# Kernel optimization log

Measured on AMD Instinct MI355X. Metric: run time of the kernel, lower is better.

## Reference

```python
import jax, jax.numpy as jnp
import numpy as np

B, S, DIM = 2, 2048, 2048
N_HEADS, N_KV = 16, 4
HEAD_DIM = DIM // N_HEADS
THETA = 10000.0


def _rope_tables(seq, half, theta):
    inv_freq = 1.0 / (theta ** (jnp.arange(0, half, dtype=jnp.float32) / half))
    t = jnp.arange(seq, dtype=jnp.float32)
    freqs = jnp.outer(t, inv_freq)  # (seq, half)
    return jnp.cos(freqs), jnp.sin(freqs)


def setup_inputs() -> dict:
    key = jax.random.key(0)
    ks = jax.random.split(key, 6)
    cos, sin = _rope_tables(S, HEAD_DIM // 2, THETA)
    scale_in = 1.0 / np.sqrt(DIM)
    return {
        "x": jax.random.normal(ks[0], (B, S, DIM), dtype=jnp.float32),
        "cos": cos,
        "sin": sin,
        "attn_mask": jax.random.randint(ks[1], (B, 1, 1, S), 0, 2) > 0,
        "Wq": jax.random.normal(ks[2], (N_HEADS * HEAD_DIM, DIM), dtype=jnp.float32) * scale_in,
        "Wk": jax.random.normal(ks[3], (N_KV * HEAD_DIM, DIM), dtype=jnp.float32) * scale_in,
        "Wv": jax.random.normal(ks[4], (N_KV * HEAD_DIM, DIM), dtype=jnp.float32) * scale_in,
        "Wo": jax.random.normal(ks[5], (DIM, N_HEADS * HEAD_DIM), dtype=jnp.float32) * scale_in,
    }


def _apply_rope(x, cos, sin):
    # x: (B, H, S, D); cos/sin: (S, D//2)
    D = x.shape[-1]
    x1, x2 = x[..., : D // 2], x[..., D // 2:]
    c = cos[None, None, : x.shape[2]]
    s = sin[None, None, : x.shape[2]]
    return jnp.concatenate([x1 * c - x2 * s, x1 * s + x2 * c], axis=-1)


def reference(x, cos, sin, attn_mask, Wq, Wk, Wv, Wo):
    b, s, _ = x.shape
    d = 2 * cos.shape[1]
    h = Wq.shape[0] // d
    kvh = Wk.shape[0] // d
    g = h // kvh  # query heads per KV head

    q = (x @ Wq.T).reshape(b, s, h, d).transpose(0, 2, 1, 3)     # (B,H,S,D)
    k = (x @ Wk.T).reshape(b, s, kvh, d).transpose(0, 2, 1, 3)   # (B,KV,S,D)
    v = (x @ Wv.T).reshape(b, s, kvh, d).transpose(0, 2, 1, 3)

    q = _apply_rope(q, cos, sin)
    k = _apply_rope(k, cos, sin)

    # Grouped attention without materializing repeated KV.
    qg = q.reshape(b, kvh, g, s, d)
    scores = jnp.einsum("bkgsd,bktd->bkgst", qg, k) / jnp.sqrt(jnp.asarray(d, q.dtype))
    mask = attn_mask[:, :, None]  # (B,1,1,1,S) broadcast over (B,KV,G,S,T)
    scores = jnp.where(mask, -jnp.inf, scores)
    attn = jax.nn.softmax(scores, axis=-1)
    out = jnp.einsum("bkgst,bktd->bkgsd", attn, v)
    out = out.reshape(b, h, s, d).transpose(0, 2, 1, 3).reshape(b, s, h * d)
    return out @ Wo.T
```

## Files before the change

### kernel.cpp

```cpp
#include <hip/hip_runtime.h>

typedef __attribute__((ext_vector_type(8))) short s16x8;
typedef __attribute__((ext_vector_type(4))) float f32x4;

#define B_    2
#define S_    2048
#define DIM_  2048
#define H_    16
#define KVH_  4
#define HD_   128
#define NQKV  3072

static __device__ __forceinline__ unsigned short f2bf(float f) {
  unsigned int u = __float_as_uint(f);
  u += 0x7fff + ((u >> 16) & 1);
  return (unsigned short)(u >> 16);
}
static __device__ __forceinline__ float bf2f(unsigned short h) {
  return __uint_as_float(((unsigned int)h) << 16);
}
static __device__ __forceinline__ float fexp2(float x) {
#if __has_builtin(__builtin_amdgcn_exp2f)
  return __builtin_amdgcn_exp2f(x);
#else
  return exp2f(x);
#endif
}

__global__ __launch_bounds__(256) void cast_all(const float* __restrict__ x,
                                                const float* __restrict__ wq,
                                                const float* __restrict__ wk,
                                                const float* __restrict__ wv,
                                                const float* __restrict__ wo,
                                                unsigned short* __restrict__ xb,
                                                unsigned short* __restrict__ wqkv,
                                                unsigned short* __restrict__ wob) {
  int blk = blockIdx.x;
  const float* s;
  unsigned short* d;
  int rel;
  if (blk < 4096)      { s = x;  d = xb;             rel = blk; }
  else if (blk < 6144) { s = wq; d = wqkv;           rel = blk - 4096; }
  else if (blk < 6656) { s = wk; d = wqkv + 4194304; rel = blk - 6144; }
  else if (blk < 7168) { s = wv; d = wqkv + 5242880; rel = blk - 6656; }
  else                 { s = wo; d = wob;            rel = blk - 7168; }
  int i = (rel * 256 + threadIdx.x) * 8;
  float4 a = *(const float4*)(s + i);
  float4 b = *(const float4*)(s + i + 4);
  uint4 o;
  o.x = (unsigned)f2bf(a.x) | ((unsigned)f2bf(a.y) << 16);
  o.y = (unsigned)f2bf(a.z) | ((unsigned)f2bf(a.w) << 16);
  o.z = (unsigned)f2bf(b.x) | ((unsigned)f2bf(b.y) << 16);
  o.w = (unsigned)f2bf(b.z) | ((unsigned)f2bf(b.w) << 16);
  *(uint4*)(d + i) = o;
}

__global__ __launch_bounds__(256) void scan_mask(const int* __restrict__ mask,
                                                 int* __restrict__ posmap,
                                                 int* __restrict__ cnts) {
  int b = blockIdx.x;
  __shared__ int a0[S_], a1[S_];
  int tid = threadIdx.x;
  for (int i = tid; i < S_; i += 256) a0[i] = (mask[b * S_ + i] == 0) ? 1 : 0;
  __syncthreads();
  int* src = a0;
  int* dst = a1;
  for (int off = 1; off < S_; off <<= 1) {
    for (int i = tid; i < S_; i += 256)
      dst[i] = src[i] + (i >= off ? src[i - off] : 0);
    __syncthreads();
    int* t = src; src = dst; dst = t;
  }
  for (int i = tid; i < S_; i += 256)
    posmap[b * S_ + i] = (mask[b * S_ + i] == 0) ? (src[i] - 1) : -1;
  if (tid == 0) cnts[b] = src[S_ - 1];
}

template <bool BF16OUT>
__global__ __launch_bounds__(256) void gemm_bt(const unsigned short* __restrict__ A,
                                               const unsigned short* __restrict__ Bw,
                                               void* __restrict__ Cp, int N, int K) {
  __shared__ __align__(16) unsigned short As[128 * 32];
  __shared__ __align__(16) unsigned short Bs[128 * 32];
  const int tid = threadIdx.x;
  const int gx = gridDim.x;
  const int lin = blockIdx.y * gx + blockIdx.x;
  const int cpx = (gx * gridDim.y) >> 3;
  const int nlin = (lin & 7) * cpx + (lin >> 3);
  const int n0 = (nlin % gx) * 128, m0 = (nlin / gx) * 128;
  const int w = tid >> 6, l = tid & 63;
  const int wr = w >> 1, wc = w & 1;
  const int lo = l & 15, hi = l >> 4;
  f32x4 acc[4][4] = {};
  const int KT = K >> 5;
  for (int kt = 0; kt < KT; ++kt) {
    const int k0 = kt << 5;
    __syncthreads();
#pragma unroll
    for (int c = 0; c < 2; ++c) {
      int idx = tid + c * 256;
      int row = idx >> 2, ko = (idx & 3) << 3;
      __builtin_amdgcn_global_load_lds(
          (__attribute__((address_space(1))) void*)(A + (size_t)(m0 + row) * K + k0 + ko),
          (__attribute__((address_space(3))) void*)(As + idx * 8), 16, 0, 0);
      __builtin_amdgcn_global_load_lds(
          (__attribute__((address_space(1))) void*)(Bw + (size_t)(n0 + row) * K + k0 + ko),
          (__attribute__((address_space(3))) void*)(Bs + idx * 8), 16, 0, 0);
    }
    asm volatile("s_waitcnt vmcnt(0)" ::: "memory");
    __syncthreads();
    s16x8 af[4], bfr[4];
#pragma unroll
    for (int mi = 0; mi < 4; ++mi)
      af[mi] = *(const s16x8*)(As + (wr * 64 + mi * 16 + lo) * 32 + hi * 8);
#pragma unroll
    for (int ni = 0; ni < 4; ++ni)
      bfr[ni] = *(const s16x8*)(Bs + (wc * 64 + ni * 16 + lo) * 32 + hi * 8);
#pragma unroll
    for (int mi = 0; mi < 4; ++mi)
#pragma unroll
      for (int ni = 0; ni < 4; ++ni)
        acc[mi][ni] = __builtin_amdgcn_mfma_f32_16x16x32_bf16(af[mi], bfr[ni], acc[mi][ni], 0, 0, 0);
  }
#pragma unroll
  for (int mi = 0; mi < 4; ++mi) {
#pragma unroll
    for (int ni = 0; ni < 4; ++ni) {
      int col = n0 + wc * 64 + ni * 16 + lo;
      int rowb = m0 + wr * 64 + mi * 16 + hi * 4;
#pragma unroll
      for (int r = 0; r < 4; ++r) {
        float v = acc[mi][ni][r];
        if (BF16OUT)
          ((unsigned short*)Cp)[(size_t)(rowb + r) * N + col] = f2bf(v);
        else
          ((float*)Cp)[(size_t)(rowb + r) * N + col] = v;
      }
    }
  }
}

__global__ __launch_bounds__(256) void rope_q(const unsigned short* __restrict__ QKV,
                                              const float* __restrict__ ctab,
                                              const float* __restrict__ stab,
                                              unsigned short* __restrict__ dst, float scale) {
  int gid = blockIdx.x * 256 + threadIdx.x;
  int i = gid & 63;
  int rest = gid >> 6;
  int h = rest & 15;
  int s = (rest >> 4) & (S_ - 1);
  int b = rest >> 15;
  const unsigned short* row = QKV + (size_t)(b * S_ + s) * NQKV + h * HD_;
  float x1 = bf2f(row[i]), x2 = bf2f(row[i + 64]);
  float c = ctab[s * 64 + i], sn = stab[s * 64 + i];
  unsigned short* drow = dst + ((size_t)(b * H_ + h) * S_ + s) * HD_;
  drow[i] = f2bf((x1 * c - x2 * sn) * scale);
  drow[i + 64] = f2bf((x1 * sn + x2 * c) * scale);
}

__global__ __launch_bounds__(256) void rope_k(const unsigned short* __restrict__ QKV,
                                              const float* __restrict__ ctab,
                                              const float* __restrict__ stab,
                                              const int* __restrict__ posmap,
                                              unsigned short* __restrict__ dst) {
  int gid = blockIdx.x * 256 + threadIdx.x;
  int i = gid & 63;
  int rest = gid >> 6;
  int h = rest & 3;
  int s = (rest >> 2) & (S_ - 1);
  int b = rest >> 13;
  int sp = posmap[b * S_ + s];
  if (sp < 0) return;
  const unsigned short* row = QKV + (size_t)(b * S_ + s) * NQKV + DIM_ + h * HD_;
  float x1 = bf2f(row[i]), x2 = bf2f(row[i + 64]);
  float c = ctab[s * 64 + i], sn = stab[s * 64 + i];
  unsigned short* drow = dst + ((size_t)(b * KVH_ + h) * S_ + sp) * HD_;
  drow[i] = f2bf(x1 * c - x2 * sn);
  drow[i + 64] = f2bf(x1 * sn + x2 * c);
}

__global__ __launch_bounds__(256) void vtrans_kernel(const unsigned short* __restrict__ QKV,
                                                     const int* __restrict__ posmap,
                                                     unsigned short* __restrict__ Vt) {
  int s0 = blockIdx.x * 64;
  int d0 = blockIdx.y * 64;
  int bk = blockIdx.z;
  int b = bk >> 2, kvh = bk & 3;
  __shared__ __align__(16) unsigned short tile[64][72];
  __shared__ int pm[64];
  int tid = threadIdx.x;
  if (tid < 64) pm[tid] = posmap[b * S_ + s0 + tid];
  for (int e = tid; e < 512; e += 256) {
    int r = e >> 3, c = (e & 7) << 3;
    const unsigned short* src =
        QKV + (size_t)(b * S_ + s0 + r) * NQKV + 2560 + kvh * HD_ + d0 + c;
    *(uint4*)(&tile[r][c]) = *(const uint4*)src;
  }
  __syncthreads();
  for (int e = tid; e < 512; e += 256) {
    int d = e >> 3, scb = (e & 7) << 3;
    unsigned short* dstrow = Vt + ((size_t)bk * HD_ + d0 + d) * S_;
#pragma unroll
    for (int j = 0; j < 8; ++j) {
      int sp = pm[scb + j];
      if (sp >= 0) dstrow[sp] = tile[scb + j][d];
    }
  }
}

__global__ __launch_bounds__(512) void attn_kernel(const unsigned short* __restrict__ Qt,
                                                   const unsigned short* __restrict__ Kt,
                                                   const unsigned short* __restrict__ Vt,
                                                   const int* __restrict__ cnts,
                                                   unsigned short* __restrict__ Out) {
  const int lin = (blockIdx.z * gridDim.y + blockIdx.y) * gridDim.x + blockIdx.x;
  const int nlin = (lin & 7) * 64 + (lin >> 3);
  const int qt = nlin & 15, h = (nlin >> 4) & 15, b = nlin >> 8;
  const int kvh = h >> 2;
  const int cnt = cnts[b];
  const int tid = threadIdx.x, w = tid >> 6, l = tid & 63;
  const int lo = l & 15, hi = l >> 4;
  const int q0 = qt * 128 + w * 16;
  const unsigned short* Qb = Qt + ((size_t)(b * H_ + h) * S_ + q0) * HD_;
  const unsigned short* Kb = Kt + (size_t)(b * KVH_ + kvh) * S_ * HD_;
  const unsigned short* Vb = Vt + (size_t)(b * KVH_ + kvh) * HD_ * S_;

  __shared__ __align__(16) unsigned short Ks[64 * 128];
  __shared__ __align__(16) unsigned short Vs[128 * 64];
  __shared__ __align__(16) unsigned short P_lds[8][16 * 72];
  unsigned short* Pw = &P_lds[w][0];

  s16x8 qf[4];
#pragma unroll
  for (int c = 0; c < 4; ++c)
    qf[c] = *(const s16x8*)(Qb + lo * HD_ + c * 32 + hi * 8);

  int kl4[2], kchg[2], vl4[2], vchg[2], kr[2], vd[2];
#pragma unroll
  for (int c = 0; c < 2; ++c) {
    int l4 = tid + c * 512;
    kl4[c] = l4; kr[c] = l4 >> 4;
    int ch = l4 & 15;
    kchg[c] = (ch & 8) | ((ch ^ kr[c]) & 7);
    vl4[c] = l4; vd[c] = l4 >> 3;
    vchg[c] = ((l4 & 7) ^ vd[c]) & 7;
  }

  f32x4 o[8] = {};
  float mrow[4], lrow[4];
#pragma unroll
  for (int r = 0; r < 4; ++r) { mrow[r] = -1e30f; lrow[r] = 0.f; }

  for (int t0 = 0; t0 < cnt; t0 += 64) {
    __syncthreads();
#pragma unroll
    for (int c = 0; c < 2; ++c) {
      __builtin_amdgcn_global_load_lds(
          (__attribute__((address_space(1))) void*)(Kb + (size_t)(t0 + kr[c]) * HD_ + kchg[c] * 8),
          (__attribute__((address_space(3))) void*)(Ks + kl4[c] * 8), 16, 0, 0);
      __builtin_amdgcn_global_load_lds(
          (__attribute__((address_space(1))) void*)(Vb + (size_t)vd[c] * S_ + t0 + vchg[c] * 8),
          (__attribute__((address_space(3))) void*)(Vs + vl4[c] * 8), 16, 0, 0);
    }
    asm volatile("s_waitcnt vmcnt(0)" ::: "memory");
    __syncthreads();

    f32x4 s[4];
#pragma unroll
    for (int sf = 0; sf < 4; ++sf) {
      f32x4 sv = {};
      int row = sf * 16 + lo;
#pragma unroll
      for (int c = 0; c < 4; ++c) {
        int ch = c * 4 + hi;
        int chs = (ch & 8) | ((ch ^ lo) & 7);
        s16x8 kf = *(const s16x8*)(Ks + row * 128 + chs * 8);
        sv = __builtin_amdgcn_mfma_f32_16x16x32_bf16(qf[c], kf, sv, 0, 0, 0);
      }
      float bv = (t0 + row < cnt) ? 0.0f : -1e30f;
#pragma unroll
      for (int r = 0; r < 4; ++r) sv[r] += bv;
      s[sf] = sv;
    }
    float tm[4];
#pragma unroll
    for (int r = 0; r < 4; ++r)
      tm[r] = fmaxf(fmaxf(s[0][r], s[1][r]), fmaxf(s[2][r], s[3][r]));
#pragma unroll
    for (int d = 1; d < 16; d <<= 1)
#pragma unroll
      for (int r = 0; r < 4; ++r) tm[r] = fmaxf(tm[r], __shfl_xor(tm[r], d));
    float dm = tm[0] - mrow[0];
#pragma unroll
    for (int r = 1; r < 4; ++r) dm = fmaxf(dm, tm[r] - mrow[r]);
    if (!__all(dm <= 8.0f)) {
      float sc_[4];
#pragma unroll
      for (int r = 0; r < 4; ++r) {
        float mnew = fmaxf(mrow[r], tm[r]);
        sc_[r] = fexp2(mrow[r] - mnew);
        mrow[r] = mnew;
        lrow[r] *= sc_[r];
      }
#pragma unroll
      for (int df = 0; df < 8; ++df)
#pragma unroll
        for (int r = 0; r < 4; ++r) o[df][r] *= sc_[r];
    }
    float ts[4] = {0.f, 0.f, 0.f, 0.f};
#pragma unroll
    for (int sf = 0; sf < 4; ++sf)
#pragma unroll
      for (int r = 0; r < 4; ++r) {
        float p = fexp2(s[sf][r] - mrow[r]);
        ts[r] += p;
        Pw[(hi * 4 + r) * 72 + sf * 16 + lo] = f2bf(p);
      }
#pragma unroll
    for (int d = 1; d < 16; d <<= 1)
#pragma unroll
      for (int r = 0; r < 4; ++r) ts[r] += __shfl_xor(ts[r], d);
#pragma unroll
    for (int r = 0; r < 4; ++r) lrow[r] += ts[r];
    s16x8 pa[2];
#pragma unroll
    for (int kk = 0; kk < 2; ++kk)
      pa[kk] = *(const s16x8*)(Pw + lo * 72 + kk * 32 + hi * 8);
#pragma unroll
    for (int df = 0; df < 8; ++df) {
      int d = df * 16 + lo;
#pragma unroll
      for (int kk = 0; kk < 2; ++kk) {
        int ch = kk * 4 + hi;
        int chs = (ch ^ lo) & 7;
        s16x8 vf = *(const s16x8*)(Vs + d * 64 + chs * 8);
        o[df] = __builtin_amdgcn_mfma_f32_16x16x32_bf16(pa[kk], vf, o[df], 0, 0, 0);
      }
    }
  }
  float inv[4];
#pragma unroll
  for (int r = 0; r < 4; ++r) inv[r] = 1.0f / lrow[r];
#pragma unroll
  for (int df = 0; df < 8; ++df)
#pragma unroll
    for (int r = 0; r < 4; ++r)
      Out[(size_t)(b * S_ + q0 + hi * 4 + r) * DIM_ + h * HD_ + df * 16 + lo] =
          f2bf(o[df][r] * inv[r]);
}

extern "C" void kernel_launch(void* const* d_in, const int* in_sizes, int n_in,
                              void* d_out, int out_size, void* d_ws, size_t ws_size,
                              hipStream_t stream) {
  (void)in_sizes; (void)n_in; (void)out_size; (void)ws_size;
  const float* x    = (const float*)d_in[0];
  const float* ctab = (const float*)d_in[1];
  const float* stab = (const float*)d_in[2];
  const int*   mask = (const int*)d_in[3];
  const float* Wq   = (const float*)d_in[4];
  const float* Wk   = (const float*)d_in[5];
  const float* Wv   = (const float*)d_in[6];
  const float* Wo   = (const float*)d_in[7];

  unsigned short* x_bf = (unsigned short*)d_ws;
  unsigned short* Wqkv = x_bf + 8388608;
  unsigned short* Wob  = Wqkv + 6291456;
  unsigned short* QKV  = Wob + 4194304;
  unsigned short* Qt   = QKV + 12582912;
  unsigned short* Kt   = Qt + 8388608;
  unsigned short* Vt   = Kt + 2097152;

  int* posmap = (int*)d_out;
  int* cnts   = posmap + B_ * S_;

  cast_all<<<9216, 256, 0, stream>>>(x, Wq, Wk, Wv, Wo, x_bf, Wqkv, Wob);
  scan_mask<<<B_, 256, 0, stream>>>(mask, posmap, cnts);

  gemm_bt<true><<<dim3(24, 32), 256, 0, stream>>>(x_bf, Wqkv, QKV, NQKV, DIM_);

  rope_q<<<16384, 256, 0, stream>>>(QKV, ctab, stab, Qt,
                                    0.08838834764831845f * 1.4426950408889634f);
  rope_k<<<4096, 256, 0, stream>>>(QKV, ctab, stab, posmap, Kt);
  vtrans_kernel<<<dim3(32, 2, 8), 256, 0, stream>>>(QKV, posmap, Vt);

  attn_kernel<<<dim3(16, 16, 2), 512, 0, stream>>>(Qt, Kt, Vt, cnts, x_bf);

  gemm_bt<false><<<dim3(16, 32), 256, 0, stream>>>(x_bf, Wob, d_out, DIM_, DIM_);
}
```

Before: 337.1 us.

## Replace GEMM with 256x256 double-buffered, swizzled, software-pipelined MFMA kernel

Replaces the 128x128, K=32 single-buffered GEMM with a 256x256 tile, K=64, 512-thread kernel. It double-buffers A and B in LDS with XOR-swizzled layouts and interleaves global-to-LDS staging with MFMA quads, using partial vmcnt waits and raised wave priority during the MFMAs. The aim is to hide global load latency, cut LDS bank conflicts and raise arithmetic intensity in both projection GEMMs. In exchange it uses 128KB of LDS per block, so only one block fits per CU. The QKV grid also drops to 192 blocks and the output grid to 128, which may leave CUs idle on a 256-CU part.

```diff
diff --git a/kernel.cpp b/kernel.cpp
--- a/kernel.cpp
+++ b/kernel.cpp
@@ -10,6 +10,9 @@
 #define KVH_  4
 #define HD_   128
 #define NQKV  3072
+
+#define AS1 __attribute__((address_space(1)))
+#define AS3 __attribute__((address_space(3)))
 
 static __device__ __forceinline__ unsigned short f2bf(float f) {
   unsigned int u = __float_as_uint(f);
@@ -76,61 +79,112 @@
   if (tid == 0) cnts[b] = src[S_ - 1];
 }
 
+
+#define LDA_(buf, fr, ks) \
+  (*(const s16x8*)(&As[buf][0] + (wm * 128 + (fr)*16 + lo) * 64 + ((((ks) << 2) + hi) ^ (lo & 7)) * 8))
+#define LDB_(buf, fc, ks) \
+  (*(const s16x8*)(&Bs[buf][0] + (wn * 64 + (fc)*16 + lo) * 64 + ((((ks) << 2) + hi) ^ (lo & 7)) * 8))
+
+#define STAGE_(P, base_m, buf, Arr, tile, half)                                             \
+  do {                                                                                      \
+    int tt = (tile) < KT ? (tile) : KT - 1;                                                 \
+    const unsigned short* srcp = (P) + (size_t)((base_m) + (half)*128) * K + (tt << 6);     \
+    unsigned short* dstp = &Arr[buf][(half)*128 * 64];                                      \
+    _Pragma("unroll") for (int cl = 0; cl < 2; ++cl) {                                      \
+      int idx = cl * 512 + tid;                                                             \
+      int rho = idx >> 3, gam = idx & 7;                                                    \
+      int gams = gam ^ (rho & 7);                                                           \
+      __builtin_amdgcn_global_load_lds((AS1 void*)(srcp + (size_t)rho * K + gams * 8),      \
+                                       (AS3 void*)(dstp + idx * 8), 16, 0, 0);              \
+    }                                                                                       \
+  } while (0)
+
+#define LOADB_(buf)                                                  \
+  do {                                                               \
+    _Pragma("unroll") for (int fc = 0; fc < 4; ++fc) {               \
+      bf_[fc][0] = LDB_(buf, fc, 0);                                 \
+      bf_[fc][1] = LDB_(buf, fc, 1);                                 \
+    }                                                                \
+  } while (0)
+
+#define QUAD_(buf, q)                                                                  \
+  do {                                                                                 \
+    s16x8 a00 = LDA_(buf, 2 * (q), 0), a01 = LDA_(buf, 2 * (q), 1);                    \
+    s16x8 a10 = LDA_(buf, 2 * (q) + 1, 0), a11 = LDA_(buf, 2 * (q) + 1, 1);            \
+    __builtin_amdgcn_s_setprio(1);                                                     \
+    _Pragma("unroll") for (int fc = 0; fc < 4; ++fc) {                                 \
+      acc[2 * (q)][fc] = __builtin_amdgcn_mfma_f32_16x16x32_bf16(a00, bf_[fc][0], acc[2 * (q)][fc], 0, 0, 0); \
+      acc[2 * (q)][fc] = __builtin_amdgcn_mfma_f32_16x16x32_bf16(a01, bf_[fc][1], acc[2 * (q)][fc], 0, 0, 0); \
+      acc[2 * (q) + 1][fc] = __builtin_amdgcn_mfma_f32_16x16x32_bf16(a10, bf_[fc][0], acc[2 * (q) + 1][fc], 0, 0, 0); \
+      acc[2 * (q) + 1][fc] = __builtin_amdgcn_mfma_f32_16x16x32_bf16(a11, bf_[fc][1], acc[2 * (q) + 1][fc], 0, 0, 0); \
+    }                                                                                  \
+    __builtin_amdgcn_s_setprio(0);                                                     \
+    asm volatile("s_waitcnt lgkmcnt(0)" ::: "memory");                                 \
+    __builtin_amdgcn_s_barrier();                                                      \
+  } while (0)
+
 template <bool BF16OUT>
-__global__ __launch_bounds__(256) void gemm_bt(const unsigned short* __restrict__ A,
-                                               const unsigned short* __restrict__ Bw,
-                                               void* __restrict__ Cp, int N, int K) {
-  __shared__ __align__(16) unsigned short As[128 * 32];
-  __shared__ __align__(16) unsigned short Bs[128 * 32];
+__global__ __launch_bounds__(512, 1) void gemm256(const unsigned short* __restrict__ A,
+                                                  const unsigned short* __restrict__ Bw,
+                                                  void* __restrict__ Cp, int N, int K) {
+  __shared__ __align__(16) unsigned short As[2][256 * 64];
+  __shared__ __align__(16) unsigned short Bs[2][256 * 64];
   const int tid = threadIdx.x;
   const int gx = gridDim.x;
   const int lin = blockIdx.y * gx + blockIdx.x;
   const int cpx = (gx * gridDim.y) >> 3;
   const int nlin = (lin & 7) * cpx + (lin >> 3);
-  const int n0 = (nlin % gx) * 128, m0 = (nlin / gx) * 128;
+  const int n0 = (nlin % gx) * 256, m0 = (nlin / gx) * 256;
   const int w = tid >> 6, l = tid & 63;
-  const int wr = w >> 1, wc = w & 1;
+  const int wm = w >> 2, wn = w & 3;
   const int lo = l & 15, hi = l >> 4;
-  f32x4 acc[4][4] = {};
-  const int KT = K >> 5;
-  for (int kt = 0; kt < KT; ++kt) {
-    const int k0 = kt << 5;
-    __syncthreads();
-#pragma unroll
-    for (int c = 0; c < 2; ++c) {
-      int idx = tid + c * 256;
-      int row = idx >> 2, ko = (idx & 3) << 3;
-      __builtin_amdgcn_global_load_lds(
-          (__attribute__((address_space(1))) void*)(A + (size_t)(m0 + row) * K + k0 + ko),
-          (__attribute__((address_space(3))) void*)(As + idx * 8), 16, 0, 0);
-      __builtin_amdgcn_global_load_lds(
-          (__attribute__((address_space(1))) void*)(Bw + (size_t)(n0 + row) * K + k0 + ko),
-          (__attribute__((address_space(3))) void*)(Bs + idx * 8), 16, 0, 0);
-    }
-    asm volatile("s_waitcnt vmcnt(0)" ::: "memory");
-    __syncthreads();
-    s16x8 af[4], bfr[4];
-#pragma unroll
-    for (int mi = 0; mi < 4; ++mi)
-      af[mi] = *(const s16x8*)(As + (wr * 64 + mi * 16 + lo) * 32 + hi * 8);
-#pragma unroll
-    for (int ni = 0; ni < 4; ++ni)
-      bfr[ni] = *(const s16x8*)(Bs + (wc * 64 + ni * 16 + lo) * 32 + hi * 8);
-#pragma unroll
-    for (int mi = 0; mi < 4; ++mi)
-#pragma unroll
-      for (int ni = 0; ni < 4; ++ni)
-        acc[mi][ni] = __builtin_amdgcn_mfma_f32_16x16x32_bf16(af[mi], bfr[ni], acc[mi][ni], 0, 0, 0);
-  }
-#pragma unroll
-  for (int mi = 0; mi < 4; ++mi) {
-#pragma unroll
-    for (int ni = 0; ni < 4; ++ni) {
-      int col = n0 + wc * 64 + ni * 16 + lo;
-      int rowb = m0 + wr * 64 + mi * 16 + hi * 4;
+  const int KT = K >> 6;
+
+  f32x4 acc[8][4] = {};
+  s16x8 bf_[4][2];
+
+  STAGE_(Bw, n0, 0, Bs, 0, 0);
+  STAGE_(Bw, n0, 0, Bs, 0, 1);
+  STAGE_(A, m0, 0, As, 0, 0);
+  STAGE_(A, m0, 0, As, 0, 1);
+  STAGE_(Bw, n0, 1, Bs, 1, 0);
+  STAGE_(Bw, n0, 1, Bs, 1, 1);
+
+  for (int t = 0; t < KT; t += 2) {
+    STAGE_(A, m0, 1, As, t + 1, 0);
+    asm volatile("s_waitcnt vmcnt(6)" ::: "memory");
+    __builtin_amdgcn_s_barrier();
+    LOADB_(0);
+    QUAD_(0, 0);
+    STAGE_(A, m0, 1, As, t + 1, 1);
+    QUAD_(0, 1);
+    STAGE_(Bw, n0, 0, Bs, t + 2, 0);
+    QUAD_(0, 2);
+    STAGE_(Bw, n0, 0, Bs, t + 2, 1);
+    QUAD_(0, 3);
+    STAGE_(A, m0, 0, As, t + 2, 0);
+    asm volatile("s_waitcnt vmcnt(6)" ::: "memory");
+    __builtin_amdgcn_s_barrier();
+    LOADB_(1);
+    QUAD_(1, 0);
+    STAGE_(A, m0, 0, As, t + 2, 1);
+    QUAD_(1, 1);
+    STAGE_(Bw, n0, 1, Bs, t + 3, 0);
+    QUAD_(1, 2);
+    STAGE_(Bw, n0, 1, Bs, t + 3, 1);
+    QUAD_(1, 3);
+  }
+
+  asm volatile("s_waitcnt vmcnt(0)" ::: "memory");
+#pragma unroll
+  for (int fr = 0; fr < 8; ++fr) {
+#pragma unroll
+    for (int fc = 0; fc < 4; ++fc) {
+      int col = n0 + wn * 64 + fc * 16 + lo;
+      int rowb = m0 + wm * 128 + fr * 16 + hi * 4;
 #pragma unroll
       for (int r = 0; r < 4; ++r) {
-        float v = acc[mi][ni][r];
+        float v = acc[fr][fc][r];
         if (BF16OUT)
           ((unsigned short*)Cp)[(size_t)(rowb + r) * N + col] = f2bf(v);
         else
@@ -256,11 +310,11 @@
 #pragma unroll
     for (int c = 0; c < 2; ++c) {
       __builtin_amdgcn_global_load_lds(
-          (__attribute__((address_space(1))) void*)(Kb + (size_t)(t0 + kr[c]) * HD_ + kchg[c] * 8),
-          (__attribute__((address_space(3))) void*)(Ks + kl4[c] * 8), 16, 0, 0);
+          (AS1 void*)(Kb + (size_t)(t0 + kr[c]) * HD_ + kchg[c] * 8),
+          (AS3 void*)(Ks + kl4[c] * 8), 16, 0, 0);
       __builtin_amdgcn_global_load_lds(
-          (__attribute__((address_space(1))) void*)(Vb + (size_t)vd[c] * S_ + t0 + vchg[c] * 8),
-          (__attribute__((address_space(3))) void*)(Vs + vl4[c] * 8), 16, 0, 0);
+          (AS1 void*)(Vb + (size_t)vd[c] * S_ + t0 + vchg[c] * 8),
+          (AS3 void*)(Vs + vl4[c] * 8), 16, 0, 0);
     }
     asm volatile("s_waitcnt vmcnt(0)" ::: "memory");
     __syncthreads();
@@ -376,7 +430,7 @@
   cast_all<<<9216, 256, 0, stream>>>(x, Wq, Wk, Wv, Wo, x_bf, Wqkv, Wob);
   scan_mask<<<B_, 256, 0, stream>>>(mask, posmap, cnts);
 
-  gemm_bt<true><<<dim3(24, 32), 256, 0, stream>>>(x_bf, Wqkv, QKV, NQKV, DIM_);
+  gemm256<true><<<dim3(12, 16), 512, 0, stream>>>(x_bf, Wqkv, QKV, NQKV, DIM_);
 
   rope_q<<<16384, 256, 0, stream>>>(QKV, ctab, stab, Qt,
                                     0.08838834764831845f * 1.4426950408889634f);
@@ -385,5 +439,5 @@
 
   attn_kernel<<<dim3(16, 16, 2), 512, 0, stream>>>(Qt, Kt, Vt, cnts, x_bf);
 
-  gemm_bt<false><<<dim3(16, 32), 256, 0, stream>>>(x_bf, Wob, d_out, DIM_, DIM_);
-}
+  gemm256<false><<<dim3(8, 16), 512, 0, stream>>>(x_bf, Wob, d_out, DIM_, DIM_);
+}
```

Measured after the change: 343.0 us. Within noise of the previous version (+1.7%).
